# Performance work log

Measured on AMD Instinct MI355X. Metric: run time of the kernel, lower is better.

## Reference

```python
import jax, jax.numpy as jnp
import numpy as np

B = 64        # graphs in batch
N = 2048      # nodes per graph (uniform -> static pooled sizes)
DEG = 16      # avg degree
E = B * N * DEG
F0 = 128      # node feature dim


def setup_inputs() -> dict:
    key = jax.random.key(0)
    ks = jax.random.split(key, 24)
    x = jax.random.normal(ks[0], (B * N, F0), dtype=jnp.float32)
    # within-graph random edges, PyG batched-graph layout (contiguous node blocks)
    loc = jax.random.randint(ks[1], (2, B, N * DEG), 0, N)
    off = (jnp.arange(B, dtype=jnp.int32) * N)[:, None]
    src = (loc[0].astype(jnp.int32) + off).reshape(-1)
    dst = (loc[1].astype(jnp.int32) + off).reshape(-1)
    g = lambda i, shp: jax.random.normal(ks[i], shp, dtype=jnp.float32) * 0.05
    return {
        'x': x, 'src': src, 'dst': dst,
        'w1l': g(2, (128, 128)), 'b1': jnp.zeros((128,), jnp.float32), 'w1r': g(3, (128, 128)), 'pw1': g(4, (128,)),
        'w2l': g(5, (128, 128)), 'b2': jnp.zeros((128,), jnp.float32), 'w2r': g(6, (128, 128)), 'pw2': g(7, (128,)),
        'w3l': g(8, (128, 128)), 'b3': jnp.zeros((128,), jnp.float32), 'w3r': g(9, (128, 128)), 'pw3': g(10, (128,)),
        'l1w': g(11, (256, 128)), 'l1b': jnp.zeros((128,), jnp.float32),
        'l2w': g(12, (128, 64)), 'l2b': jnp.zeros((64,), jnp.float32),
        'l3w': g(13, (64, 2)), 'l3b': jnp.zeros((2,), jnp.float32),
    }


def _sage(x, src, dst, em, n_nodes, Wl, b, Wr):
    # PyG SAGEConv: lin_l(mean_{j->i} x_j) + lin_r(x_i); edge mask zeroes dropped edges
    msg = x[src] * em[:, None]                                   # [E, F] gather
    agg = jax.ops.segment_sum(msg, dst, num_segments=n_nodes)
    cnt = jax.ops.segment_sum(em, dst, num_segments=n_nodes)
    mean = agg / jnp.maximum(cnt, 1.0)[:, None]
    return mean @ Wl + b + x @ Wr


def _topk_pool(x, src, dst, em, b_graphs, n_per, w):
    # PyG TopKPooling (min_score=None): score = tanh(x@w/||w||), keep top ratio per graph,
    # gate kept features by score, drop edges touching removed nodes, relabel.
    score = jnp.tanh((x @ w) / jnp.linalg.norm(w))
    k = n_per // 2                                               # ratio = 0.5
    _, idx = jax.lax.top_k(score.reshape(b_graphs, n_per), k)    # per-graph local idx
    perm = (jnp.arange(b_graphs, dtype=jnp.int32)[:, None] * n_per + idx.astype(jnp.int32)).reshape(-1)
    xn = x[perm] * score[perm][:, None]
    ntot = b_graphs * n_per
    kept = jnp.zeros((ntot,), bool).at[perm].set(True)
    newidx = jnp.zeros((ntot,), jnp.int32).at[perm].set(jnp.arange(b_graphs * k, dtype=jnp.int32))
    emn = em * kept[src].astype(em.dtype) * kept[dst].astype(em.dtype)
    return xn, newidx[src], newidx[dst], emn, k


def _readout(x, b_graphs, n_per):
    r = x.reshape(b_graphs, n_per, -1)
    return jnp.concatenate([r.max(axis=1), r.mean(axis=1)], axis=1)  # [B, 2F]


def _forward(x, src, dst, w1l, b1, w1r, pw1, w2l, b2, w2r, pw2, w3l, b3, w3r, pw3,
             l1w, l1b, l2w, l2b, l3w, l3b):
    em = jnp.ones((src.shape[0],), x.dtype)
    n = N
    h = jax.nn.relu(_sage(x, src, dst, em, B * n, w1l, b1, w1r))
    h, src, dst, em, n = _topk_pool(h, src, dst, em, B, n, pw1)
    x1 = _readout(h, B, n)
    h = jax.nn.relu(_sage(h, src, dst, em, B * n, w2l, b2, w2r))
    h, src, dst, em, n = _topk_pool(h, src, dst, em, B, n, pw2)
    x2 = _readout(h, B, n)
    h = jax.nn.relu(_sage(h, src, dst, em, B * n, w3l, b3, w3r))
    h, src, dst, em, n = _topk_pool(h, src, dst, em, B, n, pw3)
    x3 = _readout(h, B, n)
    z = x1 + x2 + x3
    z = jax.nn.relu(z @ l1w + l1b)            # dropout is identity in eval mode
    z = jax.nn.relu(z @ l2w + l2b)
    z = z @ l3w + l3b
    return jax.nn.log_softmax(z, axis=-1)


def reference(x, src, dst, w1l, b1, w1r, pw1, w2l, b2, w2r, pw2, w3l, b3, w3r, pw3,
              l1w, l1b, l2w, l2b, l3w, l3b):
    return _forward(x, src, dst, w1l, b1, w1r, pw1, w2l, b2, w2r, pw2, w3l, b3, w3r, pw3,
                    l1w, l1b, l2w, l2b, l3w, l3b)
```

## Files before the change

### kernel.cpp

```cpp
#include <hip/hip_runtime.h>
#include <cmath>

#define NT1  131072
#define ETOT 2097152
#define NB   64
#define F    128
#define CPAD 32
#define MAXBLK 32

__global__ void hist_kernel(const int* __restrict__ dst, int* __restrict__ deg) {
  int e = blockIdx.x * blockDim.x + threadIdx.x;
  if (e < ETOT) atomicAdd(&deg[dst[e]], 1);
}

__global__ void scan1_kernel(const int* __restrict__ deg, int* __restrict__ rowstart,
                             int* __restrict__ bsum) {
  __shared__ int ls[256];
  int base = blockIdx.x * 1024;
  int t = threadIdx.x;
  int i = base + t * 4;
  int a0 = deg[i], a1 = deg[i + 1], a2 = deg[i + 2], a3 = deg[i + 3];
  int s = a0 + a1 + a2 + a3;
  ls[t] = s;
  __syncthreads();
  for (int off = 1; off < 256; off <<= 1) {
    int v = (t >= off) ? ls[t - off] : 0;
    __syncthreads();
    ls[t] += v;
    __syncthreads();
  }
  int excl = ls[t] - s;
  rowstart[i]     = excl;
  rowstart[i + 1] = excl + a0;
  rowstart[i + 2] = excl + a0 + a1;
  rowstart[i + 3] = excl + a0 + a1 + a2;
  if (t == 255) bsum[blockIdx.x] = ls[255];
}

__global__ void scan2_kernel(int* __restrict__ bsum) {
  __shared__ int ls[128];
  int t = threadIdx.x;
  int v0 = bsum[t];
  ls[t] = v0;
  __syncthreads();
  for (int off = 1; off < 128; off <<= 1) {
    int v = (t >= off) ? ls[t - off] : 0;
    __syncthreads();
    ls[t] += v;
    __syncthreads();
  }
  bsum[t] = ls[t] - v0;
}

__global__ void scan3_kernel(int* __restrict__ rowstart, const int* __restrict__ bsum,
                             int* __restrict__ cursor) {
  int base = blockIdx.x * 1024;
  int off = bsum[blockIdx.x];
  int i = base + threadIdx.x * 4;
  int r0 = rowstart[i] + off, r1 = rowstart[i + 1] + off;
  int r2 = rowstart[i + 2] + off, r3 = rowstart[i + 3] + off;
  rowstart[i] = r0; rowstart[i + 1] = r1; rowstart[i + 2] = r2; rowstart[i + 3] = r3;
  cursor[i] = r0; cursor[i + 1] = r1; cursor[i + 2] = r2; cursor[i + 3] = r3;
}

__global__ void fill_kernel(const int* __restrict__ src, const int* __restrict__ dst,
                            int* __restrict__ cursor, int* __restrict__ csr) {
  int e = blockIdx.x * blockDim.x + threadIdx.x;
  if (e < ETOT) {
    int pos = atomicAdd(&cursor[dst[e]], 1);
    csr[pos] = src[e];
  }
}

__global__ void init_id_kernel(int* __restrict__ m, int* __restrict__ orig,
                               const int* __restrict__ rowstart,
                               const int* __restrict__ deg, int2* __restrict__ sd2) {
  int v = blockIdx.x * blockDim.x + threadIdx.x;
  m[v] = v; orig[v] = v;
  sd2[v] = make_int2(rowstart[v], deg[v]);
}

template <int MAP>
__global__ __launch_bounds__(256) void agg_kernel(
    const float* __restrict__ xin, const int* __restrict__ ids,
    const int* __restrict__ m, const int2* __restrict__ sd2,
    float* __restrict__ agg, const float* __restrict__ pw,
    float* __restrict__ invn) {
  if (blockIdx.x == 0 && threadIdx.x < 64) {
    int l = threadIdx.x;
    float vv = pw[l] * pw[l] + pw[l + 64] * pw[l + 64];
    #pragma unroll
    for (int o = 32; o; o >>= 1) vv += __shfl_xor(vv, o);
    if (l == 0) *invn = 1.0f / sqrtf(vv);
  }
  int swz = gridDim.x >> 3;
  int nb  = (blockIdx.x & 7) * swz + (blockIdx.x >> 3);
  int g = threadIdx.x >> 5, l = threadIdx.x & 31;
  int jd = nb * 8 + g;
  int2 sdv = sd2[jd];
  int s = sdv.x, d = sdv.y;
  float4 acc = make_float4(0.f, 0.f, 0.f, 0.f);
  int c = 0;
  for (int base = 0; base < d; base += 32) {
    int dc = min(32, d - base);
    int nbid = -1;
    if (l < dc) {
      int e = __builtin_nontemporal_load(&ids[s + base + l]);
      nbid = MAP ? m[e] : e;
    }
    int j = 0;
    for (; j + 8 <= dc; j += 8) {
      int n[8];
      float4 v[8];
      #pragma unroll
      for (int q = 0; q < 8; ++q) n[q] = __shfl(nbid, j + q, 32);
      #pragma unroll
      for (int q = 0; q < 8; ++q)
        v[q] = *(const float4*)(xin + (size_t)max(n[q], 0) * F + l * 4);
      #pragma unroll
      for (int q = 0; q < 8; ++q)
        if (n[q] >= 0) { acc.x += v[q].x; acc.y += v[q].y; acc.z += v[q].z; acc.w += v[q].w; ++c; }
    }
    for (; j + 4 <= dc; j += 4) {
      int n0 = __shfl(nbid, j, 32);
      int n1 = __shfl(nbid, j + 1, 32);
      int n2 = __shfl(nbid, j + 2, 32);
      int n3 = __shfl(nbid, j + 3, 32);
      float4 v0 = *(const float4*)(xin + (size_t)max(n0, 0) * F + l * 4);
      float4 v1 = *(const float4*)(xin + (size_t)max(n1, 0) * F + l * 4);
      float4 v2 = *(const float4*)(xin + (size_t)max(n2, 0) * F + l * 4);
      float4 v3 = *(const float4*)(xin + (size_t)max(n3, 0) * F + l * 4);
      if (n0 >= 0) { acc.x += v0.x; acc.y += v0.y; acc.z += v0.z; acc.w += v0.w; ++c; }
      if (n1 >= 0) { acc.x += v1.x; acc.y += v1.y; acc.z += v1.z; acc.w += v1.w; ++c; }
      if (n2 >= 0) { acc.x += v2.x; acc.y += v2.y; acc.z += v2.z; acc.w += v2.w; ++c; }
      if (n3 >= 0) { acc.x += v3.x; acc.y += v3.y; acc.z += v3.z; acc.w += v3.w; ++c; }
    }
    for (; j < dc; ++j) {
      int n0 = __shfl(nbid, j, 32);
      if (n0 >= 0) {
        float4 v0 = *(const float4*)(xin + (size_t)n0 * F + l * 4);
        acc.x += v0.x; acc.y += v0.y; acc.z += v0.z; acc.w += v0.w; ++c;
      }
    }
  }
  float inv = 1.0f / (float)max(c, 1);
  acc.x *= inv; acc.y *= inv; acc.z *= inv; acc.w *= inv;
  *(float4*)(agg + (size_t)jd * F + l * 4) = acc;
}

template <int BM>
__global__ __launch_bounds__(256) void sage_gemm(
    const float* agg, const float* __restrict__ x,
    const float* __restrict__ Wl, const float* __restrict__ Wr,
    const float* __restrict__ bias, float* h,
    const float* __restrict__ pw, const float* __restrict__ invn,
    float* __restrict__ score) {
  constexpr int RQ = BM / 64;
  __shared__ float At[16][BM + 4];
  __shared__ float Wt[16][132];
  int t  = threadIdx.x;
  int tx = t & 15, ty = t >> 4;
  int i0 = blockIdx.x * BM;
  int arow, akc;
  if (BM == 128) { arow = t & 127; akc = (t >> 7) * 8; }
  else           { arow = t & 63;  akc = (t >> 6) * 4; }
  int wkr = t >> 4, wc0 = (t & 15) * 8;

  float acc[4 * RQ][8];
  #pragma unroll
  for (int r = 0; r < 4 * RQ; ++r)
    #pragma unroll
    for (int c = 0; c < 8; ++c) acc[r][c] = 0.f;

  for (int kt = 0; kt < 16; ++kt) {
    const float* Asrc = (kt < 8) ? agg : x;
    int acol = (kt & 7) * 16 + akc;
    const float* pA = Asrc + (size_t)(i0 + arow) * F + acol;
    float4 va0 = *(const float4*)pA;
    float4 va1;
    if (BM == 128) va1 = *(const float4*)(pA + 4);
    const float* Wsrc = ((kt < 8) ? Wl : Wr) + (size_t)((kt & 7) * 16 + wkr) * F + wc0;
    float4 vw0 = *(const float4*)Wsrc;
    float4 vw1 = *(const float4*)(Wsrc + 4);
    __syncthreads();
    At[akc + 0][arow] = va0.x; At[akc + 1][arow] = va0.y;
    At[akc + 2][arow] = va0.z; At[akc + 3][arow] = va0.w;
    if (BM == 128) {
      At[akc + 4][arow] = va1.x; At[akc + 5][arow] = va1.y;
      At[akc + 6][arow] = va1.z; At[akc + 7][arow] = va1.w;
    }
    *(float4*)(&Wt[wkr][wc0]) = vw0;
    *(float4*)(&Wt[wkr][wc0 + 4]) = vw1;
    __syncthreads();
    #pragma unroll
    for (int k = 0; k < 16; ++k) {
      float4 a0 = *(float4*)(&At[k][ty * 4]);
      float4 w0 = *(float4*)(&Wt[k][tx * 4]);
      float4 w1 = *(float4*)(&Wt[k][64 + tx * 4]);
      float wr[8] = {w0.x, w0.y, w0.z, w0.w, w1.x, w1.y, w1.z, w1.w};
      float ar0[4] = {a0.x, a0.y, a0.z, a0.w};
      #pragma unroll
      for (int r = 0; r < 4; ++r)
        #pragma unroll
        for (int c = 0; c < 8; ++c)
          acc[r][c] += ar0[r] * wr[c];
      if (RQ == 2) {
        float4 a1 = *(float4*)(&At[k][64 + ty * 4]);
        float ar1[4] = {a1.x, a1.y, a1.z, a1.w};
        #pragma unroll
        for (int r = 0; r < 4; ++r)
          #pragma unroll
          for (int c = 0; c < 8; ++c)
            acc[4 + r][c] += ar1[r] * wr[c];
      }
    }
  }

  float4 bb0 = *(const float4*)(bias + tx * 4);
  float4 bb1 = *(const float4*)(bias + 64 + tx * 4);
  float4 pw0 = *(const float4*)(pw + tx * 4);
  float4 pw1 = *(const float4*)(pw + 64 + tx * 4);
  float inorm = *invn;
  #pragma unroll
  for (int r = 0; r < 4 * RQ; ++r) {
    int row = i0 + ((r < 4) ? (ty * 4 + r) : (64 + ty * 4 + r - 4));
    float4 o0, o1;
    o0.x = fmaxf(acc[r][0] + bb0.x, 0.f);
    o0.y = fmaxf(acc[r][1] + bb0.y, 0.f);
    o0.z = fmaxf(acc[r][2] + bb0.z, 0.f);
    o0.w = fmaxf(acc[r][3] + bb0.w, 0.f);
    o1.x = fmaxf(acc[r][4] + bb1.x, 0.f);
    o1.y = fmaxf(acc[r][5] + bb1.y, 0.f);
    o1.z = fmaxf(acc[r][6] + bb1.z, 0.f);
    o1.w = fmaxf(acc[r][7] + bb1.w, 0.f);
    *(float4*)(h + (size_t)row * F + tx * 4) = o0;
    *(float4*)(h + (size_t)row * F + 64 + tx * 4) = o1;
    float p = o0.x * pw0.x + o0.y * pw0.y + o0.z * pw0.z + o0.w * pw0.w
            + o1.x * pw1.x + o1.y * pw1.y + o1.z * pw1.z + o1.w * pw1.w;
    #pragma unroll
    for (int off = 8; off; off >>= 1) p += __shfl_xor(p, off);
    if (tx == 0) score[row] = tanhf(p * inorm);
  }
}

__global__ __launch_bounds__(256) void topk_kernel(
    const float* __restrict__ score, float* __restrict__ thr,
    int* __restrict__ quota, int* __restrict__ tiecur,
    int* __restrict__ curg, int nper, int k) {
  __shared__ unsigned su[2048];
  __shared__ int hist[256];
  __shared__ int vsel;
  int b = blockIdx.x, t = threadIdx.x;
  for (int i = t; i < nper; i += 256) {
    unsigned u = __float_as_uint(score[b * nper + i]);
    su[i] = (u & 0x80000000u) ? ~u : (u | 0x80000000u);
  }
  __syncthreads();
  unsigned prefix = 0;
  int rem = k;
  for (int shift = 24; shift >= 0; shift -= 8) {
    hist[t] = 0;
    __syncthreads();
    unsigned maskhi = (shift == 24) ? 0u : (0xFFFFFFFFu << (shift + 8));
    for (int i = t; i < nper; i += 256) {
      unsigned u = su[i];
      if ((u & maskhi) == prefix) atomicAdd(&hist[(u >> shift) & 255], 1);
    }
    __syncthreads();
    for (int off = 1; off < 256; off <<= 1) {
      int v = (t + off < 256) ? hist[t + off] : 0;
      __syncthreads();
      hist[t] += v;
      __syncthreads();
    }
    if (hist[t] >= rem && (t == 255 || hist[t + 1] < rem)) vsel = t;
    __syncthreads();
    int v = vsel;
    int above = (v == 255) ? 0 : hist[v + 1];
    rem -= above;
    prefix |= ((unsigned)v << shift);
    __syncthreads();
  }
  if (t == 0) {
    unsigned s = prefix;
    unsigned ub = (s >> 31) ? (s & 0x7FFFFFFFu) : ~s;
    thr[b] = __uint_as_float(ub);
    quota[b] = rem;
    tiecur[b * CPAD] = 0; curg[b * CPAD] = 0;
  }
}

__global__ __launch_bounds__(256) void select_kernel(
    const float* __restrict__ h, const float* __restrict__ score,
    const float* __restrict__ thr, const int* __restrict__ quota,
    int* __restrict__ tiecur, int* __restrict__ curg,
    const int* __restrict__ origA, int* __restrict__ origB,
    int* __restrict__ m, float* __restrict__ xnext,
    const int* __restrict__ rowstart, const int* __restrict__ deg,
    int2* __restrict__ sd2, float* __restrict__ pmax, float* __restrict__ psum,
    int nper, int k) {
  __shared__ int   snid[64];
  __shared__ float ssc[64];
  __shared__ float smax[8][128], ssum[8][128];
  int t = threadIdx.x;
  int base = blockIdx.x * 64;
  int b = base / nper;
  if (t < 64) {
    int i = base + t;
    float sc = score[i];
    float T = thr[b];
    int keep = (sc > T) ? 1 : 0;
    if (!keep && sc == T) keep = (atomicAdd(&tiecur[b * CPAD], 1) < quota[b]) ? 1 : 0;
    unsigned long long mask = __ballot(keep);
    int pre = __popcll(mask & ((1ull << t) - 1ull));
    int tot = __popcll(mask);
    int wbase = 0;
    if (t == 0 && tot) wbase = atomicAdd(&curg[b * CPAD], tot);
    wbase = __shfl(wbase, 0);
    int nid = keep ? (b * k + wbase + pre) : -1;
    int orig = origA[i];
    m[orig] = nid;
    if (nid >= 0) {
      origB[nid] = orig;
      sd2[nid] = make_int2(rowstart[orig], deg[orig]);
    }
    snid[t] = nid; ssc[t] = sc;
  }
  __syncthreads();
  int g = t >> 5, l32 = t & 31;
  float4 pm = make_float4(-INFINITY, -INFINITY, -INFINITY, -INFINITY);
  float4 ps = make_float4(0.f, 0.f, 0.f, 0.f);
  for (int n = g; n < 64; n += 8) {
    int nid = snid[n];
    if (nid >= 0) {
      float sc = ssc[n];
      float4 v = *(const float4*)(h + (size_t)(base + n) * F + l32 * 4);
      v.x *= sc; v.y *= sc; v.z *= sc; v.w *= sc;
      *(float4*)(xnext + (size_t)nid * F + l32 * 4) = v;
      pm.x = fmaxf(pm.x, v.x); pm.y = fmaxf(pm.y, v.y);
      pm.z = fmaxf(pm.z, v.z); pm.w = fmaxf(pm.w, v.w);
      ps.x += v.x; ps.y += v.y; ps.z += v.z; ps.w += v.w;
    }
  }
  *(float4*)(&smax[g][l32 * 4]) = pm;
  *(float4*)(&ssum[g][l32 * 4]) = ps;
  __syncthreads();
  if (t < 128) {
    float mx = -INFINITY, sm = 0.f;
    #pragma unroll
    for (int gg = 0; gg < 8; ++gg) {
      mx = fmaxf(mx, smax[gg][t]);
      sm += ssum[gg][t];
    }
    int nblk = nper >> 6;
    int blkpos = blockIdx.x - b * nblk;
    int o = (b * MAXBLK + blkpos) * 128 + t;
    pmax[o] = mx; psum[o] = sm;
  }
}

__global__ void mlp_kernel(const float* __restrict__ pmax,
                           const float* __restrict__ psum,
                           const float* __restrict__ l1w, const float* __restrict__ l1b,
                           const float* __restrict__ l2w, const float* __restrict__ l2b,
                           const float* __restrict__ l3w, const float* __restrict__ l3b,
                           float* __restrict__ out) {
  int b = blockIdx.x, t = threadIdx.x;
  __shared__ float zz[256], o1[128], o2[64], lg[2];
  const int nblk3[3] = {32, 16, 8};
  const float invk3[3] = {1.0f / 1024.f, 1.0f / 512.f, 1.0f / 256.f};
  float summax = 0.f, summean = 0.f;
  #pragma unroll
  for (int s = 0; s < 3; ++s) {
    const float* pm = pmax + (size_t)s * NB * MAXBLK * F;
    const float* ps = psum + (size_t)s * NB * MAXBLK * F;
    float mx = -INFINITY, sm = 0.f;
    for (int ch = 0; ch < nblk3[s]; ++ch) {
      int o = (b * MAXBLK + ch) * 128 + t;
      mx = fmaxf(mx, pm[o]);
      sm += ps[o];
    }
    summax += mx;
    summean += sm * invk3[s];
  }
  zz[t] = summax;
  zz[t + 128] = summean;
  __syncthreads();
  float a = l1b[t];
  for (int i = 0; i < 256; ++i) a += zz[i] * l1w[i * 128 + t];
  o1[t] = fmaxf(a, 0.f);
  __syncthreads();
  if (t < 64) {
    float a2 = l2b[t];
    for (int i = 0; i < 128; ++i) a2 += o1[i] * l2w[i * 64 + t];
    o2[t] = fmaxf(a2, 0.f);
  }
  __syncthreads();
  if (t < 2) {
    float a3 = l3b[t];
    for (int i = 0; i < 64; ++i) a3 += o2[i] * l3w[i * 2 + t];
    lg[t] = a3;
  }
  __syncthreads();
  if (t == 0) {
    float mmax = fmaxf(lg[0], lg[1]);
    float lse = mmax + logf(expf(lg[0] - mmax) + expf(lg[1] - mmax));
    out[b * 2 + 0] = lg[0] - lse;
    out[b * 2 + 1] = lg[1] - lse;
  }
}

extern "C" void kernel_launch(void* const* d_in, const int* in_sizes, int n_in,
                              void* d_out, int out_size, void* d_ws, size_t ws_size,
                              hipStream_t stream) {
  const float* x   = (const float*)d_in[0];
  const int*   src = (const int*)d_in[1];
  const int*   dst = (const int*)d_in[2];
  const float* Wl[3] = {(const float*)d_in[3], (const float*)d_in[7],  (const float*)d_in[11]};
  const float* bs[3] = {(const float*)d_in[4], (const float*)d_in[8],  (const float*)d_in[12]};
  const float* Wr[3] = {(const float*)d_in[5], (const float*)d_in[9],  (const float*)d_in[13]};
  const float* pw[3] = {(const float*)d_in[6], (const float*)d_in[10], (const float*)d_in[14]};
  const float* l1w = (const float*)d_in[15]; const float* l1b = (const float*)d_in[16];
  const float* l2w = (const float*)d_in[17]; const float* l2b = (const float*)d_in[18];
  const float* l3w = (const float*)d_in[19]; const float* l3b = (const float*)d_in[20];
  float* out = (float*)d_out;

  char* p = (char*)d_ws;
  auto take = [&](size_t bytes) { char* q = p; p += (bytes + 255) & ~(size_t)255; return q; };
  float* aggh   = (float*)take((size_t)NT1 * F * 4);
  float* xbuf   = (float*)take((size_t)65536 * F * 4);
  float* score  = (float*)take((size_t)NT1 * 4);
  int* deg      = (int*)take((size_t)NT1 * 4);
  int* rowstart = (int*)take((size_t)NT1 * 4);
  int* cursor   = (int*)take((size_t)NT1 * 4);
  int* m        = (int*)take((size_t)NT1 * 4);
  int* origA    = (int*)take((size_t)NT1 * 4);
  int* origB    = (int*)take((size_t)NT1 * 4);
  int2* sd2     = (int2*)take((size_t)NT1 * 8);
  int* csr      = (int*)take((size_t)ETOT * 4);
  int* bsum     = (int*)take(128 * 4);
  float* thr    = (float*)take(NB * 4);
  int* quota    = (int*)take(NB * 4);
  int* tiecur   = (int*)take(NB * CPAD * 4);
  int* curg     = (int*)take(NB * CPAD * 4);
  float* pmax   = (float*)take((size_t)3 * NB * MAXBLK * F * 4);
  float* psum   = (float*)take((size_t)3 * NB * MAXBLK * F * 4);
  float* invn   = (float*)take(4);

  hipMemsetAsync(deg, 0, (size_t)NT1 * 4, stream);

  hist_kernel<<<ETOT / 256, 256, 0, stream>>>(dst, deg);
  scan1_kernel<<<128, 256, 0, stream>>>(deg, rowstart, bsum);
  scan2_kernel<<<1, 128, 0, stream>>>(bsum);
  scan3_kernel<<<128, 256, 0, stream>>>(rowstart, bsum, cursor);
  fill_kernel<<<ETOT / 256, 256, 0, stream>>>(src, dst, cursor, csr);
  init_id_kernel<<<NT1 / 256, 256, 0, stream>>>(m, origA, rowstart, deg, sd2);

  int NT = NT1, nper = 2048;
  const float* xin = x;
  int* oin = origA; int* oout = origB;
  for (int s = 0; s < 3; ++s) {
    int k = nper / 2;
    float* pmaxS = pmax + (size_t)s * NB * MAXBLK * F;
    float* psumS = psum + (size_t)s * NB * MAXBLK * F;
    if (s == 0)
      agg_kernel<0><<<NT / 8, 256, 0, stream>>>(xin, csr, m, sd2, aggh, pw[s], invn);
    else
      agg_kernel<1><<<NT / 8, 256, 0, stream>>>(xin, csr, m, sd2, aggh, pw[s], invn);
    if (s == 0)
      sage_gemm<128><<<NT / 128, 256, 0, stream>>>(aggh, xin, Wl[s], Wr[s], bs[s], aggh,
                                                   pw[s], invn, score);
    else
      sage_gemm<64><<<NT / 64, 256, 0, stream>>>(aggh, xin, Wl[s], Wr[s], bs[s], aggh,
                                                 pw[s], invn, score);
    topk_kernel<<<NB, 256, 0, stream>>>(score, thr, quota, tiecur, curg, nper, k);
    select_kernel<<<NT / 64, 256, 0, stream>>>(aggh, score, thr, quota, tiecur, curg,
                                               oin, oout, m, xbuf, rowstart, deg, sd2,
                                               pmaxS, psumS, nper, k);
    NT = NB * k; nper = k; xin = xbuf;
    int* tmp = oin; oin = oout; oout = tmp;
  }
  mlp_kernel<<<NB, 128, 0, stream>>>(pmax, psum, l1w, l1b, l2w, l2b, l3w, l3b, out);
}
```

Before: 662.8 us.

## Fuse neighbor mean aggregation into SAGE GEMM via shared-memory tile

Merges the separate aggregation kernel and the SAGE GEMM kernel into one kernel per layer. Each 64-node block gathers neighbor means into a transposed shared-memory tile and feeds it straight into the Wl half of the GEMM. The x half is still loaded from global memory. This removes the round trip of the aggregated features through global memory and one launch per layer. In exchange it uses about 45KB of shared memory per block, which may lower occupancy. It also drops the block-index swizzle and the 128-row GEMM tile for layer 1.

```diff
diff --git a/kernel.cpp b/kernel.cpp
--- a/kernel.cpp
+++ b/kernel.cpp
@@ -81,120 +81,117 @@
 }
 
 template <int MAP>
-__global__ __launch_bounds__(256) void agg_kernel(
+__global__ __launch_bounds__(256) void sage_fused(
     const float* __restrict__ xin, const int* __restrict__ ids,
     const int* __restrict__ m, const int2* __restrict__ sd2,
-    float* __restrict__ agg, const float* __restrict__ pw,
-    float* __restrict__ invn) {
-  if (blockIdx.x == 0 && threadIdx.x < 64) {
-    int l = threadIdx.x;
-    float vv = pw[l] * pw[l] + pw[l + 64] * pw[l + 64];
+    const float* __restrict__ Wl, const float* __restrict__ Wr,
+    const float* __restrict__ bias, float* __restrict__ h,
+    const float* __restrict__ pw, float* __restrict__ score) {
+  __shared__ float meanT[128][68];
+  __shared__ float At[16][68];
+  __shared__ float Wt[16][132];
+  __shared__ float s_inorm;
+  int t = threadIdx.x;
+  int tx = t & 15, ty = t >> 4;
+  int i0 = blockIdx.x * 64;
+
+  if (t < 64) {
+    float vv = pw[t] * pw[t] + pw[t + 64] * pw[t + 64];
     #pragma unroll
     for (int o = 32; o; o >>= 1) vv += __shfl_xor(vv, o);
-    if (l == 0) *invn = 1.0f / sqrtf(vv);
-  }
-  int swz = gridDim.x >> 3;
-  int nb  = (blockIdx.x & 7) * swz + (blockIdx.x >> 3);
-  int g = threadIdx.x >> 5, l = threadIdx.x & 31;
-  int jd = nb * 8 + g;
-  int2 sdv = sd2[jd];
-  int s = sdv.x, d = sdv.y;
-  float4 acc = make_float4(0.f, 0.f, 0.f, 0.f);
-  int c = 0;
-  for (int base = 0; base < d; base += 32) {
-    int dc = min(32, d - base);
-    int nbid = -1;
-    if (l < dc) {
-      int e = __builtin_nontemporal_load(&ids[s + base + l]);
-      nbid = MAP ? m[e] : e;
-    }
-    int j = 0;
-    for (; j + 8 <= dc; j += 8) {
-      int n[8];
-      float4 v[8];
-      #pragma unroll
-      for (int q = 0; q < 8; ++q) n[q] = __shfl(nbid, j + q, 32);
-      #pragma unroll
-      for (int q = 0; q < 8; ++q)
-        v[q] = *(const float4*)(xin + (size_t)max(n[q], 0) * F + l * 4);
-      #pragma unroll
-      for (int q = 0; q < 8; ++q)
-        if (n[q] >= 0) { acc.x += v[q].x; acc.y += v[q].y; acc.z += v[q].z; acc.w += v[q].w; ++c; }
-    }
-    for (; j + 4 <= dc; j += 4) {
-      int n0 = __shfl(nbid, j, 32);
-      int n1 = __shfl(nbid, j + 1, 32);
-      int n2 = __shfl(nbid, j + 2, 32);
-      int n3 = __shfl(nbid, j + 3, 32);
-      float4 v0 = *(const float4*)(xin + (size_t)max(n0, 0) * F + l * 4);
-      float4 v1 = *(const float4*)(xin + (size_t)max(n1, 0) * F + l * 4);
-      float4 v2 = *(const float4*)(xin + (size_t)max(n2, 0) * F + l * 4);
-      float4 v3 = *(const float4*)(xin + (size_t)max(n3, 0) * F + l * 4);
-      if (n0 >= 0) { acc.x += v0.x; acc.y += v0.y; acc.z += v0.z; acc.w += v0.w; ++c; }
-      if (n1 >= 0) { acc.x += v1.x; acc.y += v1.y; acc.z += v1.z; acc.w += v1.w; ++c; }
-      if (n2 >= 0) { acc.x += v2.x; acc.y += v2.y; acc.z += v2.z; acc.w += v2.w; ++c; }
-      if (n3 >= 0) { acc.x += v3.x; acc.y += v3.y; acc.z += v3.z; acc.w += v3.w; ++c; }
-    }
-    for (; j < dc; ++j) {
-      int n0 = __shfl(nbid, j, 32);
-      if (n0 >= 0) {
-        float4 v0 = *(const float4*)(xin + (size_t)n0 * F + l * 4);
-        acc.x += v0.x; acc.y += v0.y; acc.z += v0.z; acc.w += v0.w; ++c;
+    if (t == 0) s_inorm = 1.0f / sqrtf(vv);
+  }
+
+  {
+    int g = t >> 5, l = t & 31;
+    for (int lr = g; lr < 64; lr += 8) {
+      int2 sdv = sd2[i0 + lr];
+      int s = sdv.x, d = sdv.y;
+      float4 acc = make_float4(0.f, 0.f, 0.f, 0.f);
+      int c = 0;
+      for (int base = 0; base < d; base += 32) {
+        int dc = min(32, d - base);
+        int nbid = -1;
+        if (l < dc) {
+          int e = __builtin_nontemporal_load(&ids[s + base + l]);
+          nbid = MAP ? m[e] : e;
+        }
+        int j = 0;
+        for (; j + 8 <= dc; j += 8) {
+          int n[8];
+          float4 v[8];
+          #pragma unroll
+          for (int q = 0; q < 8; ++q) n[q] = __shfl(nbid, j + q, 32);
+          #pragma unroll
+          for (int q = 0; q < 8; ++q)
+            v[q] = *(const float4*)(xin + (size_t)max(n[q], 0) * F + l * 4);
+          #pragma unroll
+          for (int q = 0; q < 8; ++q)
+            if (n[q] >= 0) { acc.x += v[q].x; acc.y += v[q].y; acc.z += v[q].z; acc.w += v[q].w; ++c; }
+        }
+        for (; j + 4 <= dc; j += 4) {
+          int n0 = __shfl(nbid, j, 32);
+          int n1 = __shfl(nbid, j + 1, 32);
+          int n2 = __shfl(nbid, j + 2, 32);
+          int n3 = __shfl(nbid, j + 3, 32);
+          float4 v0 = *(const float4*)(xin + (size_t)max(n0, 0) * F + l * 4);
+          float4 v1 = *(const float4*)(xin + (size_t)max(n1, 0) * F + l * 4);
+          float4 v2 = *(const float4*)(xin + (size_t)max(n2, 0) * F + l * 4);
+          float4 v3 = *(const float4*)(xin + (size_t)max(n3, 0) * F + l * 4);
+          if (n0 >= 0) { acc.x += v0.x; acc.y += v0.y; acc.z += v0.z; acc.w += v0.w; ++c; }
+          if (n1 >= 0) { acc.x += v1.x; acc.y += v1.y; acc.z += v1.z; acc.w += v1.w; ++c; }
+          if (n2 >= 0) { acc.x += v2.x; acc.y += v2.y; acc.z += v2.z; acc.w += v2.w; ++c; }
+          if (n3 >= 0) { acc.x += v3.x; acc.y += v3.y; acc.z += v3.z; acc.w += v3.w; ++c; }
+        }
+        for (; j < dc; ++j) {
+          int n0 = __shfl(nbid, j, 32);
+          if (n0 >= 0) {
+            float4 v0 = *(const float4*)(xin + (size_t)n0 * F + l * 4);
+            acc.x += v0.x; acc.y += v0.y; acc.z += v0.z; acc.w += v0.w; ++c;
+          }
+        }
       }
-    }
-  }
-  float inv = 1.0f / (float)max(c, 1);
-  acc.x *= inv; acc.y *= inv; acc.z *= inv; acc.w *= inv;
-  *(float4*)(agg + (size_t)jd * F + l * 4) = acc;
-}
-
-template <int BM>
-__global__ __launch_bounds__(256) void sage_gemm(
-    const float* agg, const float* __restrict__ x,
-    const float* __restrict__ Wl, const float* __restrict__ Wr,
-    const float* __restrict__ bias, float* h,
-    const float* __restrict__ pw, const float* __restrict__ invn,
-    float* __restrict__ score) {
-  constexpr int RQ = BM / 64;
-  __shared__ float At[16][BM + 4];
-  __shared__ float Wt[16][132];
-  int t  = threadIdx.x;
-  int tx = t & 15, ty = t >> 4;
-  int i0 = blockIdx.x * BM;
-  int arow, akc;
-  if (BM == 128) { arow = t & 127; akc = (t >> 7) * 8; }
-  else           { arow = t & 63;  akc = (t >> 6) * 4; }
+      float inv = 1.0f / (float)max(c, 1);
+      meanT[l * 4 + 0][lr] = acc.x * inv;
+      meanT[l * 4 + 1][lr] = acc.y * inv;
+      meanT[l * 4 + 2][lr] = acc.z * inv;
+      meanT[l * 4 + 3][lr] = acc.w * inv;
+    }
+  }
+  __syncthreads();
+
+  int arow = t & 63, akc = (t >> 6) * 4;
   int wkr = t >> 4, wc0 = (t & 15) * 8;
 
-  float acc[4 * RQ][8];
+  float acc[4][8];
   #pragma unroll
-  for (int r = 0; r < 4 * RQ; ++r)
+  for (int r = 0; r < 4; ++r)
     #pragma unroll
     for (int c = 0; c < 8; ++c) acc[r][c] = 0.f;
 
   for (int kt = 0; kt < 16; ++kt) {
-    const float* Asrc = (kt < 8) ? agg : x;
-    int acol = (kt & 7) * 16 + akc;
-    const float* pA = Asrc + (size_t)(i0 + arow) * F + acol;
-    float4 va0 = *(const float4*)pA;
-    float4 va1;
-    if (BM == 128) va1 = *(const float4*)(pA + 4);
-    const float* Wsrc = ((kt < 8) ? Wl : Wr) + (size_t)((kt & 7) * 16 + wkr) * F + wc0;
+    bool xhalf = (kt >= 8);
+    float4 va0;
+    if (xhalf) {
+      int acol = (kt & 7) * 16 + akc;
+      va0 = *(const float4*)(xin + (size_t)(i0 + arow) * F + acol);
+    }
+    const float* Wsrc = (xhalf ? Wr : Wl) + (size_t)((kt & 7) * 16 + wkr) * F + wc0;
     float4 vw0 = *(const float4*)Wsrc;
     float4 vw1 = *(const float4*)(Wsrc + 4);
     __syncthreads();
-    At[akc + 0][arow] = va0.x; At[akc + 1][arow] = va0.y;
-    At[akc + 2][arow] = va0.z; At[akc + 3][arow] = va0.w;
-    if (BM == 128) {
-      At[akc + 4][arow] = va1.x; At[akc + 5][arow] = va1.y;
-      At[akc + 6][arow] = va1.z; At[akc + 7][arow] = va1.w;
+    if (xhalf) {
+      At[akc + 0][arow] = va0.x; At[akc + 1][arow] = va0.y;
+      At[akc + 2][arow] = va0.z; At[akc + 3][arow] = va0.w;
     }
     *(float4*)(&Wt[wkr][wc0]) = vw0;
     *(float4*)(&Wt[wkr][wc0 + 4]) = vw1;
     __syncthreads();
+    const float (*Ap)[68] = xhalf ? (const float (*)[68])At
+                                  : (const float (*)[68])&meanT[kt * 16];
     #pragma unroll
     for (int k = 0; k < 16; ++k) {
-      float4 a0 = *(float4*)(&At[k][ty * 4]);
+      float4 a0 = *(const float4*)(&Ap[k][ty * 4]);
       float4 w0 = *(float4*)(&Wt[k][tx * 4]);
       float4 w1 = *(float4*)(&Wt[k][64 + tx * 4]);
       float wr[8] = {w0.x, w0.y, w0.z, w0.w, w1.x, w1.y, w1.z, w1.w};
@@ -204,15 +201,6 @@
         #pragma unroll
         for (int c = 0; c < 8; ++c)
           acc[r][c] += ar0[r] * wr[c];
-      if (RQ == 2) {
-        float4 a1 = *(float4*)(&At[k][64 + ty * 4]);
-        float ar1[4] = {a1.x, a1.y, a1.z, a1.w};
-        #pragma unroll
-        for (int r = 0; r < 4; ++r)
-          #pragma unroll
-          for (int c = 0; c < 8; ++c)
-            acc[4 + r][c] += ar1[r] * wr[c];
-      }
     }
   }
 
@@ -220,10 +208,10 @@
   float4 bb1 = *(const float4*)(bias + 64 + tx * 4);
   float4 pw0 = *(const float4*)(pw + tx * 4);
   float4 pw1 = *(const float4*)(pw + 64 + tx * 4);
-  float inorm = *invn;
+  float inorm = s_inorm;
   #pragma unroll
-  for (int r = 0; r < 4 * RQ; ++r) {
-    int row = i0 + ((r < 4) ? (ty * 4 + r) : (64 + ty * 4 + r - 4));
+  for (int r = 0; r < 4; ++r) {
+    int row = i0 + ty * 4 + r;
     float4 o0, o1;
     o0.x = fmaxf(acc[r][0] + bb0.x, 0.f);
     o0.y = fmaxf(acc[r][1] + bb0.y, 0.f);
@@ -427,7 +415,7 @@
 
   char* p = (char*)d_ws;
   auto take = [&](size_t bytes) { char* q = p; p += (bytes + 255) & ~(size_t)255; return q; };
-  float* aggh   = (float*)take((size_t)NT1 * F * 4);
+  float* h      = (float*)take((size_t)NT1 * F * 4);
   float* xbuf   = (float*)take((size_t)65536 * F * 4);
   float* score  = (float*)take((size_t)NT1 * 4);
   int* deg      = (int*)take((size_t)NT1 * 4);
@@ -445,7 +433,6 @@
   int* curg     = (int*)take(NB * CPAD * 4);
   float* pmax   = (float*)take((size_t)3 * NB * MAXBLK * F * 4);
   float* psum   = (float*)take((size_t)3 * NB * MAXBLK * F * 4);
-  float* invn   = (float*)take(4);
 
   hipMemsetAsync(deg, 0, (size_t)NT1 * 4, stream);
 
@@ -464,17 +451,13 @@
     float* pmaxS = pmax + (size_t)s * NB * MAXBLK * F;
     float* psumS = psum + (size_t)s * NB * MAXBLK * F;
     if (s == 0)
-      agg_kernel<0><<<NT / 8, 256, 0, stream>>>(xin, csr, m, sd2, aggh, pw[s], invn);
+      sage_fused<0><<<NT / 64, 256, 0, stream>>>(xin, csr, m, sd2, Wl[s], Wr[s], bs[s],
+                                                 h, pw[s], score);
     else
-      agg_kernel<1><<<NT / 8, 256, 0, stream>>>(xin, csr, m, sd2, aggh, pw[s], invn);
-    if (s == 0)
-      sage_gemm<128><<<NT / 128, 256, 0, stream>>>(aggh, xin, Wl[s], Wr[s], bs[s], aggh,
-                                                   pw[s], invn, score);
-    else
-      sage_gemm<64><<<NT / 64, 256, 0, stream>>>(aggh, xin, Wl[s], Wr[s], bs[s], aggh,
-                                                 pw[s], invn, score);
+      sage_fused<1><<<NT / 64, 256, 0, stream>>>(xin, csr, m, sd2, Wl[s], Wr[s], bs[s],
+                                                 h, pw[s], score);
     topk_kernel<<<NB, 256, 0, stream>>>(score, thr, quota, tiecur, curg, nper, k);
-    select_kernel<<<NT / 64, 256, 0, stream>>>(aggh, score, thr, quota, tiecur, curg,
+    select_kernel<<<NT / 64, 256, 0, stream>>>(h, score, thr, quota, tiecur, curg,
                                                oin, oout, m, xbuf, rowstart, deg, sd2,
                                                pmaxS, psumS, nper, k);
     NT = NB * k; nper = k; xin = xbuf;
```

Result: slower. 808.1 us (+21.9%).
